# Kernel optimization log

Measured on AMD Instinct MI355X. Metric: run time of the kernel, lower is better.

## Reference

```python
import jax, jax.numpy as jnp
import numpy as np

EPS = 1e-5  # torch BatchNorm1d default eps
NH, KD, D_V = 8, 64, 128  # num_heads, key_dim, per-head value dim (attn_ratio*key_dim)


def hardswish(x):
    return x * jnp.clip(x + 3.0, 0.0, 6.0) / 6.0


def linear_bn(x, W, g, b):
    # Linear (no bias) followed by BatchNorm1d in training mode: batch stats
    # over all leading dims (torch flattens (B,N) before BN).
    y = x @ W.T
    yf = y.reshape(-1, y.shape[-1])
    mu = yf.mean(0)
    var = yf.var(0)  # biased variance, matching BN normalization
    return (y - mu) * (g / jnp.sqrt(var + EPS)) + b


def setup_inputs() -> dict:
    key = jax.random.key(0)
    ks = jax.random.split(key, 22)
    B, C, H, W, NT, D = 8, 1024, 96, 96, 60, 512
    dh = NH * D_V          # 1024
    h_kv = dh + NH * KD    # 1536
    hf = 2 * D             # 1024 (mr=2)

    def p(k, shape, s=0.02):
        return jax.random.normal(k, shape, jnp.float32) * s

    return {
        "im_emd": jax.random.normal(ks[0], (B, C, H, W), jnp.float32),
        "text_emd": jax.random.normal(ks[1], (NT, D), jnp.float32),
        "W_dc": p(ks[2], (D, C)), "g_dc": 1.0 + p(ks[3], (D,)), "b_dc": p(ks[4], (D,)),
        "W_kv": p(ks[5], (h_kv, D)), "g_kv": 1.0 + p(ks[6], (h_kv,)), "b_kv": p(ks[7], (h_kv,)),
        "W_q": p(ks[8], (NH * KD, D)), "g_q": 1.0 + p(ks[9], (NH * KD,)), "b_q": p(ks[10], (NH * KD,)),
        "W_proj": p(ks[11], (D, dh)), "g_proj": 1.0 + p(ks[12], (D,)), "b_proj": p(ks[13], (D,)),
        "biases": p(ks[14], (NH, 10000)),  # relative-position bias table (100x100 offsets)
        "W_f1": p(ks[15], (hf, D)), "g_f1": 1.0 + p(ks[16], (hf,)), "b_f1": p(ks[17], (hf,)),
        "W_f2": p(ks[18], (D, hf)), "g_f2": 1.0 + p(ks[19], (D,)), "b_f2": p(ks[20], (D,)),
    }


def _bias_idx(NT, H, W):
    # Offset table built row-major over product(range(100), range(100)) =>
    # attention_offsets[(a,b)] == 100*a + b. Text token t maps to grid point
    # (t//100, t%100); image token n to (n//W, n%W).
    t = np.arange(NT)
    n = np.arange(H * W)
    dx = np.abs(t[:, None] // 100 - n[None, :] // W)
    dy = np.abs(t[:, None] % 100 - n[None, :] % W)
    return 100 * dx + dy  # [NT, N]


def reference(im_emd, text_emd, W_dc, g_dc, b_dc, W_kv, g_kv, b_kv,
              W_q, g_q, b_q, W_proj, g_proj, b_proj, biases,
              W_f1, g_f1, b_f1, W_f2, g_f2, b_f2):
    B, C, H, W = im_emd.shape
    N = H * W
    NT, D = text_emd.shape
    dh = NH * D_V
    scale = KD ** -0.5

    # image tokens -> embed_dim
    x = im_emd.reshape(B, C, N).transpose(0, 2, 1)          # [B,N,C]
    xd = hardswish(linear_bn(x, W_dc, g_dc, b_dc))          # [B,N,D]

    # Attentioninv: text queries attend over image keys/values
    kv = linear_bn(xd, W_kv, g_kv, b_kv).reshape(B, N, NH, KD + D_V)
    k, v = kv[..., :KD], kv[..., KD:]                       # [B,N,h,64], [B,N,h,128]
    q = linear_bn(text_emd[None], W_q, g_q, b_q).reshape(NT, NH, KD)  # [NT,h,64]

    idx = jnp.asarray(_bias_idx(NT, H, W))                  # [NT,N] static
    bias = biases[:, idx]                                   # [h,NT,N] gather

    attn = jnp.einsum('thd,bnhd->bhtn', q, k) * scale + bias[None]
    attn = jax.nn.softmax(attn, axis=-1)                    # [B,h,NT,N]
    out = jnp.einsum('bhtn,bnhd->bthd', attn, v).reshape(B, NT, dh)
    out = linear_bn(hardswish(out), W_proj, g_proj, b_proj)  # [B,NT,D]

    textd = text_emd[None] + out                            # residual (broadcast)

    # ffntext: Linear_BN -> Hardswish -> Linear_BN(bn_weight_init=0) + residual
    f = hardswish(linear_bn(textd, W_f1, g_f1, b_f1))
    f = linear_bn(f, W_f2, g_f2, b_f2)
    textd = f + textd
    return textd[0]  # [NT, D]
```

## Files before the change

kernel.cpp:

```cpp
#include <hip/hip_runtime.h>
#include <hip/hip_bf16.h>
#include <stdint.h>

typedef short bf16x8 __attribute__((ext_vector_type(8)));
typedef float f32x4 __attribute__((ext_vector_type(4)));

__device__ __forceinline__ float b2f(ushort u){ return __uint_as_float(((uint32_t)u)<<16); }
__device__ __forceinline__ ushort f2b(float f){
  uint32_t u = __float_as_uint(f);
  u += 0x7fffu + ((u>>16)&1u);
  return (ushort)(u>>16);
}
__device__ __forceinline__ float hswish(float x){ return x*fminf(fmaxf(x+3.f,0.f),6.f)*(1.f/6.f); }

__device__ __forceinline__ void gll16(const void* g, void* l){
  __builtin_amdgcn_global_load_lds((const __attribute__((address_space(1))) void*)g,
                                   (__attribute__((address_space(3))) void*)l, 16, 0, 0);
}

__global__ void init_kernel(const float* __restrict__ Wdc, const float* __restrict__ Wkv,
                            ushort* __restrict__ Wdc_b, ushort* __restrict__ Wkv_b,
                            float* __restrict__ zbase){
  int i = blockIdx.x*256 + threadIdx.x;
  if (i < 8192) zbase[i] = 0.f;
  for (int j=i; j<512*1024; j+=262144) Wdc_b[j] = f2b(Wdc[j]);
  for (int j=i; j<1536*512; j+=262144) Wkv_b[j] = f2b(Wkv[j]);
}

__global__ __launch_bounds__(256) void transpose_kernel(const float* __restrict__ im, ushort* __restrict__ At){
  __shared__ float tb[64][65];
  const int b = blockIdx.z, c0 = blockIdx.y*64, n0 = blockIdx.x*64;
  const int tid = threadIdx.x;
  const int cl = tid >> 2, q = tid & 3;
  #pragma unroll
  for (int it=0; it<4; ++it){
    int nn = q*4 + it*16;
    float4 v = *(const float4*)&im[((size_t)(b*1024 + c0 + cl))*9216 + n0 + nn];
    tb[cl][nn+0]=v.x; tb[cl][nn+1]=v.y; tb[cl][nn+2]=v.z; tb[cl][nn+3]=v.w;
  }
  __syncthreads();
  const int nr = tid >> 4, c4 = (tid & 15)*4;
  #pragma unroll
  for (int ps=0; ps<4; ++ps){
    int nn = nr + ps*16;
    ushort4 u;
    u.x = f2b(tb[c4+0][nn]); u.y = f2b(tb[c4+1][nn]);
    u.z = f2b(tb[c4+2][nn]); u.w = f2b(tb[c4+3][nn]);
    *(ushort4*)&At[((size_t)(b*9216 + n0 + nn))*1024 + c0 + c4] = u;
  }
}

template<int SPLIT>
__global__ __launch_bounds__(256) void gemm_bt(
    const ushort* __restrict__ A, const ushort* __restrict__ Bm,
    ushort* __restrict__ Cm, ushort* __restrict__ Vt,
    float* __restrict__ sums, float* __restrict__ sqs,
    int NT, int N, int K)
{
  __shared__ __align__(16) ushort As[128*64];
  __shared__ __align__(16) ushort Bs[128*64];
  const int tid = threadIdx.x;
  const int l = tid & 63;
  const int w = tid >> 6;
  const int wm = w >> 1, wn = w & 1;
  const int chunk = gridDim.x >> 3;
  const int wg = (blockIdx.x & 7)*chunk + (blockIdx.x >> 3);
  const int tn = wg % NT, tm = wg / NT;
  const size_t n0 = (size_t)tn * 128;
  const size_t m0 = (size_t)tm * 128;
  const int lr = l & 15, lk = l >> 4;
  const int wbase = tid & ~63;

  const ushort* asrc[4]; const ushort* bsrc[4]; ushort* adst[4]; ushort* bdst[4];
  #pragma unroll
  for (int it=0; it<4; ++it){
    int idx = it*256 + tid;
    int row = idx >> 3, c8 = idx & 7;
    int sc8 = c8 ^ (row & 7);
    asrc[it] = A  + (m0+row)*K + sc8*8;
    bsrc[it] = Bm + (n0+row)*K + sc8*8;
    adst[it] = &As[(it*256 + wbase)*8];
    bdst[it] = &Bs[(it*256 + wbase)*8];
  }
  const int swz = (lr & 7) << 3;
  const ushort* ap0 = &As[(wm*64 + lr)*64 + ((lk*8) ^ swz)];
  const ushort* ap1 = &As[(wm*64 + lr)*64 + ((lk*8) ^ swz ^ 32)];
  const ushort* bp0 = &Bs[(wn*64 + lr)*64 + ((lk*8) ^ swz)];
  const ushort* bp1 = &Bs[(wn*64 + lr)*64 + ((lk*8) ^ swz ^ 32)];

  f32x4 acc[4][4];
  #pragma unroll
  for (int i=0;i<4;++i)
    #pragma unroll
    for (int j=0;j<4;++j) acc[i][j] = (f32x4){0.f,0.f,0.f,0.f};

  for (int kt = 0; kt < K; kt += 64) {
    #pragma unroll
    for (int it=0; it<4; ++it) {
      gll16(asrc[it] + kt, adst[it]);
      gll16(bsrc[it] + kt, bdst[it]);
    }
    __syncthreads();
    #pragma unroll
    for (int kk=0; kk<2; ++kk) {
      const ushort* ap = kk ? ap1 : ap0;
      const ushort* bp = kk ? bp1 : bp0;
      bf16x8 af[4], bfr[4];
      #pragma unroll
      for (int i=0;i<4;++i) af[i]  = *(const bf16x8*)(ap + i*1024);
      #pragma unroll
      for (int j=0;j<4;++j) bfr[j] = *(const bf16x8*)(bp + j*1024);
      #pragma unroll
      for (int i=0;i<4;++i)
        #pragma unroll
        for (int j=0;j<4;++j)
          acc[i][j] = __builtin_amdgcn_mfma_f32_16x16x32_bf16(af[i], bfr[j], acc[i][j], 0, 0, 0);
    }
    __syncthreads();
  }
  if constexpr (SPLIT==0){
    #pragma unroll
    for (int i=0;i<4;++i)
      #pragma unroll
      for (int j=0;j<4;++j)
        #pragma unroll
        for (int r=0;r<4;++r) {
          size_t row = m0 + wm*64 + i*16 + lk*4 + r;
          size_t col = n0 + wn*64 + j*16 + lr;
          Cm[row*N + col] = f2b(acc[i][j][r]);
        }
  } else {
    const int bq = (int)(m0/9216);
    const int nbase = (int)(m0 - (size_t)bq*9216);
    #pragma unroll
    for (int j=0;j<4;++j){
      int c = (int)n0 + wn*64 + j*16 + lr;
      int h = c/192, rcol = c - h*192;
      #pragma unroll
      for (int i=0;i<4;++i){
        int nrow = nbase + wm*64 + i*16 + lk*4;
        if (rcol < 64){
          ushort* kb = Cm + ((size_t)(bq*9216 + nrow))*512 + h*64 + rcol;
          #pragma unroll
          for (int r=0;r<4;++r) kb[(size_t)r*512] = f2b(acc[i][j][r]);
        } else {
          int dv = rcol - 64;
          ushort4 u;
          u.x=f2b(acc[i][j][0]); u.y=f2b(acc[i][j][1]);
          u.z=f2b(acc[i][j][2]); u.w=f2b(acc[i][j][3]);
          *(ushort4*)&Vt[((size_t)((bq*8+h)*128 + dv))*9216 + nrow] = u;
        }
      }
    }
  }
  #pragma unroll
  for (int j=0;j<4;++j){
    float cs=0.f, cq=0.f;
    #pragma unroll
    for (int i=0;i<4;++i)
      #pragma unroll
      for (int r=0;r<4;++r){ float v=acc[i][j][r]; cs+=v; cq+=v*v; }
    cs += __shfl_xor(cs,16); cs += __shfl_xor(cs,32);
    cq += __shfl_xor(cq,16); cq += __shfl_xor(cq,32);
    if (lk==0){
      int col = (int)n0 + wn*64 + j*16 + lr;
      atomicAdd(&sums[col], cs);
      atomicAdd(&sqs [col], cq);
    }
  }
}

__global__ __launch_bounds__(256) void bn_hswish(ushort* __restrict__ y,
    const float* __restrict__ ssum, const float* __restrict__ ssq,
    const float* __restrict__ g, const float* __restrict__ bb)
{
  __shared__ float sc[512], sh[512];
  const float invn = 1.f/73728.f;
  for (int i=threadIdx.x;i<512;i+=256){
    float mu = ssum[i]*invn;
    float var = ssq[i]*invn - mu*mu;
    float k = g[i]*rsqrtf(var+1e-5f);
    sc[i]=k; sh[i]=bb[i]-mu*k;
  }
  __syncthreads();
  const size_t total = (size_t)73728*512/8;
  for (size_t idx = (size_t)blockIdx.x*256+threadIdx.x; idx < total; idx += (size_t)gridDim.x*256){
    uint4 u = *(uint4*)&y[idx*8];
    ushort* up = (ushort*)&u;
    int c0 = ((int)(idx & 63))*8;
    #pragma unroll
    for (int e=0;e<8;++e){
      float x = b2f(up[e])*sc[c0+e] + sh[c0+e];
      up[e] = f2b(hswish(x));
    }
    *(uint4*)&y[idx*8] = u;
  }
}

__global__ __launch_bounds__(256) void q_gemm(const float* __restrict__ text, const float* __restrict__ Wq, float* __restrict__ qraw)
{
  __shared__ __align__(16) float xr[512];
  const int t = blockIdx.x, tid = threadIdx.x;
  for (int i=tid;i<512;i+=256) xr[i] = text[t*512+i];
  __syncthreads();
  #pragma unroll
  for (int cj=0;cj<2;++cj){
    int c = cj*256+tid;
    const float4* wp = (const float4*)(Wq + (size_t)c*512);
    const float4* xp = (const float4*)xr;
    float a=0.f;
    for (int u=0;u<128;++u){
      float4 wv = wp[u], xv = xp[u];
      a += wv.x*xv.x + wv.y*xv.y + wv.z*xv.z + wv.w*xv.w;
    }
    qraw[t*512+c]=a;
  }
}

__global__ __launch_bounds__(512) void q_bn_qh(const float* __restrict__ qraw,
                                               const float* __restrict__ g, const float* __restrict__ bb,
                                               const float* __restrict__ s2sum, const float* __restrict__ s2sq,
                                               const float* __restrict__ g_kv, const float* __restrict__ b_kv,
                                               ushort* __restrict__ Qh, float* __restrict__ cQ)
{
  const int c = threadIdx.x;
  const int h = c >> 6, d = c & 63;
  float s=0.f,q=0.f;
  for (int t=0;t<60;++t){ float v = qraw[t*512+c]; s+=v; q+=v*v; }
  float mu=s*(1.f/60.f), var=q*(1.f/60.f)-mu*mu;
  float k = g[c]*rsqrtf(var+1e-5f);
  float sh = bb[c]-mu*k;
  const float invn = 1.f/73728.f;
  float mu2 = s2sum[h*192+d]*invn;
  float var2 = s2sq[h*192+d]*invn - mu2*mu2;
  float k2 = g_kv[h*192+d]*rsqrtf(var2+1e-5f);
  const float sk = k2*0.125f;
  const float tk = (b_kv[h*192+d]-mu2*k2)*0.125f;
  for (int t=0;t<60;++t){
    float qv = qraw[t*512+c]*k+sh;
    Qh[(h*64+t)*64+d] = f2b(qv*sk);
    float contrib = qv*tk;
    #pragma unroll
    for (int o=32;o>0;o>>=1) contrib += __shfl_xor(contrib,o);
    if (d==0) cQ[h*64+t] = contrib;
  }
  for (int t=60;t<64;++t) Qh[(h*64+t)*64+d] = 0;
  if (d==0) for (int t=60;t<64;++t) cQ[h*64+t] = 0.f;
}

__global__ __launch_bounds__(256) void attn_flash(
    const ushort* __restrict__ Qh, const float* __restrict__ cQ,
    const ushort* __restrict__ Kbuf, const ushort* __restrict__ Vt,
    const float* __restrict__ biases,
    float* __restrict__ Op, float* __restrict__ Mp, float* __restrict__ Lp)
{
  __shared__ __align__(16) ushort Qs[64*72];
  __shared__ __align__(16) ushort vt[128*64];
  __shared__ __align__(16) ushort Pw[4][16*72];
  __shared__ float bias_l[600];
  __shared__ float cQs[64];
  const int tid = threadIdx.x;
  const int l = tid & 63, w = tid >> 6;
  const int lr = l & 15, lk = l >> 4;
  const int nc = blockIdx.x, h = blockIdx.y, b = blockIdx.z;
  const int bh = b*8+h;
  const int wbase = tid & ~63;
  for (int cid = tid; cid < 512; cid += 256){
    int row = cid >> 3, c8 = cid & 7;
    *(uint4*)&Qs[row*72 + c8*8] = *(const uint4*)&Qh[(size_t)(h*64+row)*64 + c8*8];
  }
  for (int i = tid; i < 600; i += 256) bias_l[i] = biases[h*10000 + nc*600 + i];
  if (tid < 64) cQs[tid] = cQ[h*64 + tid];

  const ushort* vsrc0 = Vt + (size_t)bh*128*9216 + nc*576;
  const ushort* vsrc[4]; ushort* vdst[4];
  #pragma unroll
  for (int it=0; it<4; ++it){
    int idx = it*256 + tid;
    int row = idx >> 3, c8 = idx & 7;
    int sc8 = c8 ^ (row & 7);
    vsrc[it] = vsrc0 + (size_t)row*9216 + sc8*8;
    vdst[it] = &vt[(it*256 + wbase)*8];
  }
  const int swz = (lr & 7) << 3;
  const ushort* vp0 = &vt[lr*64 + ((lk*8) ^ swz)];
  const ushort* vp1 = &vt[lr*64 + ((lk*8) ^ swz ^ 32)];
  const ushort* kchunk = Kbuf + (size_t)b*9216*512 + h*64;
  const ushort* qsp = &Qs[(w*16+lr)*72 + lk*8];
  const ushort* pwp = &Pw[w][lr*72 + lk*8];

  float m_run[4] = {-1e30f,-1e30f,-1e30f,-1e30f};
  float l_run[4] = {0.f,0.f,0.f,0.f};
  f32x4 acc_o[8];
  #pragma unroll
  for (int j=0;j<8;++j) acc_o[j] = (f32x4){0.f,0.f,0.f,0.f};
  __syncthreads();

  for (int tile=0; tile<9; ++tile){
    const int n0 = nc*576 + tile*64;
    if (tile) __syncthreads();
    #pragma unroll
    for (int it=0; it<4; ++it) gll16(vsrc[it] + tile*64, vdst[it]);
    __syncthreads();
    f32x4 sa[4];
    #pragma unroll
    for (int j=0;j<4;++j) sa[j]=(f32x4){0.f,0.f,0.f,0.f};
    const ushort* kbase = kchunk + (size_t)n0*512;
    __builtin_amdgcn_s_setprio(1);
    #pragma unroll
    for (int kk=0; kk<64; kk+=32){
      bf16x8 af = *(const bf16x8*)(qsp + kk);
      #pragma unroll
      for (int j=0;j<4;++j){
        bf16x8 bf_ = *(const bf16x8*)&kbase[(size_t)(j*16+lr)*512 + kk + lk*8];
        sa[j] = __builtin_amdgcn_mfma_f32_16x16x32_bf16(af, bf_, sa[j], 0,0,0);
      }
    }
    __builtin_amdgcn_s_setprio(0);
    float mt[4] = {-1e30f,-1e30f,-1e30f,-1e30f};
    #pragma unroll
    for (int j=0;j<4;++j){
      int n = n0 + j*16 + lr;
      int py = n/96;
      int px = n - py*96;
      int pyl = py - nc*6;
      #pragma unroll
      for (int r=0;r<4;++r){
        int t = w*16 + lk*4 + r;
        int dd = t - px; dd = dd<0?-dd:dd;
        float s = sa[j][r] + cQs[t] + bias_l[pyl*100 + dd];
        sa[j][r] = s;
        mt[r] = fmaxf(mt[r], s);
      }
    }
    #pragma unroll
    for (int r=0;r<4;++r){
      #pragma unroll
      for (int o=1;o<16;o<<=1) mt[r] = fmaxf(mt[r], __shfl_xor(mt[r], o));
      float mnew = fmaxf(m_run[r], mt[r]);
      float ef = __expf(m_run[r] - mnew);
      m_run[r] = mnew;
      l_run[r] *= ef;
      #pragma unroll
      for (int j2=0;j2<8;++j2) acc_o[j2][r] *= ef;
    }
    float rs[4] = {0.f,0.f,0.f,0.f};
    #pragma unroll
    for (int j=0;j<4;++j)
      #pragma unroll
      for (int r=0;r<4;++r){
        float pe = __expf(sa[j][r] - m_run[r]);
        rs[r] += pe;
        Pw[w][(lk*4+r)*72 + j*16 + lr] = f2b(pe);
      }
    #pragma unroll
    for (int r=0;r<4;++r){
      #pragma unroll
      for (int o=1;o<16;o<<=1) rs[r] += __shfl_xor(rs[r], o);
      l_run[r] += rs[r];
    }
    __builtin_amdgcn_s_setprio(1);
    #pragma unroll
    for (int kk=0; kk<2; ++kk){
      bf16x8 pa = *(const bf16x8*)(pwp + kk*32);
      const ushort* vp = kk ? vp1 : vp0;
      #pragma unroll
      for (int j2=0;j2<8;++j2){
        bf16x8 vb = *(const bf16x8*)(vp + j2*1024);
        acc_o[j2] = __builtin_amdgcn_mfma_f32_16x16x32_bf16(pa, vb, acc_o[j2], 0,0,0);
      }
    }
    __builtin_amdgcn_s_setprio(0);
  }
  float* ob = Op + (((size_t)nc*64 + bh)*64)*128;
  #pragma unroll
  for (int j2=0;j2<8;++j2)
    #pragma unroll
    for (int r=0;r<4;++r){
      int row = w*16 + lk*4 + r;
      ob[(size_t)row*128 + j2*16 + lr] = acc_o[j2][r];
    }
  if (lr == 0){
    #pragma unroll
    for (int r=0;r<4;++r){
      int row = w*16 + lk*4 + r;
      Mp[(nc*64+bh)*64 + row] = m_run[r];
      Lp[(nc*64+bh)*64 + row] = l_run[r];
    }
  }
}

__global__ __launch_bounds__(128) void attn_combine(
    const float* __restrict__ Op, const float* __restrict__ Mp, const float* __restrict__ Lp,
    float* __restrict__ attn_o)
{
  const int t = blockIdx.x, bh = blockIdx.y;
  const int b = bh >> 3, h = bh & 7;
  const int dv = threadIdx.x;
  float mv[16];
  float m_g = -1e30f;
  #pragma unroll
  for (int i=0;i<16;++i){ mv[i] = Mp[(i*64+bh)*64 + t]; m_g = fmaxf(m_g, mv[i]); }
  float lsum = 0.f;
  #pragma unroll
  for (int i=0;i<16;++i) lsum += Lp[(i*64+bh)*64 + t] * __expf(mv[i]-m_g);
  float o = 0.f;
  #pragma unroll
  for (int i=0;i<16;++i)
    o += Op[(((size_t)i*64 + bh)*64 + t)*128 + dv] * __expf(mv[i]-m_g);
  attn_o[(size_t)(b*60+t)*1024 + h*128 + dv] = o / lsum;
}

template<int CIN, int COUT, int MODE>
__global__ __launch_bounds__(256) void rowgemm8(
    const float* __restrict__ X, const float* __restrict__ Wt,
    const float* __restrict__ isum, const float* __restrict__ isq,
    const float* __restrict__ ig, const float* __restrict__ ib, float invn,
    const float* __restrict__ text, float* __restrict__ textd,
    float* __restrict__ out, float* __restrict__ osum, float* __restrict__ osq)
{
  __shared__ __align__(16) float xr[8][CIN];
  __shared__ float scf[CIN], shf[CIN];
  const int rb0 = blockIdx.x*8, tid = threadIdx.x;
  for (int i=tid; i<CIN; i+=256){
    int idx = (MODE==3) ? (64 + (i&127) + (i>>7)*192) : i;
    float mu = isum[idx]*invn;
    float var = isq[idx]*invn - mu*mu;
    float k = ig[idx]*rsqrtf(var+1e-5f);
    scf[i]=k; shf[i]=ib[idx]-mu*k;
  }
  __syncthreads();
  for (int i=tid; i<8*CIN; i+=256){
    int rr = i / CIN, cc = i % CIN;
    float v = X[(size_t)(rb0+rr)*CIN + cc];
    v = v*scf[cc] + shf[cc];
    if constexpr (MODE==2 || MODE==3) v = hswish(v);
    if constexpr (MODE==4){
      int t = (rb0+rr) % 60;
      v = text[t*CIN+cc] + v;
      if (blockIdx.y == 0) textd[(size_t)(rb0+rr)*CIN + cc] = v;
    }
    xr[rr][cc]=v;
  }
  __syncthreads();
  int c = blockIdx.y*256 + tid;
  const float4* wp = (const float4*)(Wt + (size_t)c*CIN);
  float a[8] = {0.f,0.f,0.f,0.f,0.f,0.f,0.f,0.f};
  for (int u=0;u<CIN/4;++u){
    float4 wv = wp[u];
    #pragma unroll
    for (int rr=0;rr<8;++rr){
      float4 xv = *(const float4*)&xr[rr][u*4];
      a[rr] += wv.x*xv.x + wv.y*xv.y + wv.z*xv.z + wv.w*xv.w;
    }
  }
  float ps=0.f, pq=0.f;
  #pragma unroll
  for (int rr=0;rr<8;++rr){
    out[(size_t)(rb0+rr)*COUT + c] = a[rr];
    ps += a[rr]; pq += a[rr]*a[rr];
  }
  atomicAdd(&osum[c], ps);
  atomicAdd(&osq [c], pq);
}

__global__ void final_out(const float* __restrict__ f2raw,
                          const float* __restrict__ ssum, const float* __restrict__ ssq,
                          const float* __restrict__ g, const float* __restrict__ bb,
                          const float* __restrict__ textd, float* __restrict__ outp)
{
  int i = blockIdx.x*256+threadIdx.x;
  if (i < 60*512){
    int c = i & 511;
    float mu = ssum[c]*(1.f/480.f);
    float var = ssq[c]*(1.f/480.f) - mu*mu;
    float k = g[c]*rsqrtf(var+1e-5f);
    outp[i] = f2raw[i]*k + (bb[c]-mu*k) + textd[i];
  }
}

extern "C" void kernel_launch(void* const* d_in, const int* in_sizes, int n_in,
                              void* d_out, int out_size, void* d_ws, size_t ws_size,
                              hipStream_t stream)
{
  (void)in_sizes; (void)n_in; (void)out_size; (void)ws_size;
  const float* im    = (const float*)d_in[0];
  const float* text  = (const float*)d_in[1];
  const float* W_dc  = (const float*)d_in[2];
  const float* g_dc  = (const float*)d_in[3];
  const float* b_dc  = (const float*)d_in[4];
  const float* W_kv  = (const float*)d_in[5];
  const float* g_kv  = (const float*)d_in[6];
  const float* b_kv  = (const float*)d_in[7];
  const float* W_q   = (const float*)d_in[8];
  const float* g_q   = (const float*)d_in[9];
  const float* b_q   = (const float*)d_in[10];
  const float* W_proj= (const float*)d_in[11];
  const float* g_proj= (const float*)d_in[12];
  const float* b_proj= (const float*)d_in[13];
  const float* biases= (const float*)d_in[14];
  const float* W_f1  = (const float*)d_in[15];
  const float* g_f1  = (const float*)d_in[16];
  const float* b_f1  = (const float*)d_in[17];
  const float* W_f2  = (const float*)d_in[18];
  const float* g_f2  = (const float*)d_in[19];
  const float* b_f2  = (const float*)d_in[20];
  float* outp = (float*)d_out;

  char* p = (char*)d_ws;
  auto alloc = [&](size_t bytes)->char*{ char* r = p; p += (bytes+255)&~(size_t)255; return r; };
  float* s1_sum = (float*)alloc(512*4);
  float* s1_sq  = (float*)alloc(512*4);
  float* s2_sum = (float*)alloc(1536*4);
  float* s2_sq  = (float*)alloc(1536*4);
  float* s3_sum = (float*)alloc(512*4);
  float* s3_sq  = (float*)alloc(512*4);
  float* s4_sum = (float*)alloc(1024*4);
  float* s4_sq  = (float*)alloc(1024*4);
  float* s5_sum = (float*)alloc(512*4);
  float* s5_sq  = (float*)alloc(512*4);
  float* zero_base = s1_sum;
  float* attn_o = (float*)alloc((size_t)480*1024*4);
  float* qraw = (float*)alloc(60*512*4);
  ushort* Qh = (ushort*)alloc((size_t)8*64*64*2);
  float* cQ = (float*)alloc(512*4);
  float* proj_raw = (float*)alloc((size_t)480*512*4);
  float* textd=(float*)alloc((size_t)480*512*4);
  float* f1_raw=(float*)alloc((size_t)480*1024*4);
  float* f2_raw=(float*)alloc((size_t)480*512*4);
  float* Op = (float*)alloc((size_t)16*64*64*128*4);
  float* Mp = (float*)alloc((size_t)16*64*64*4);
  float* Lp = (float*)alloc((size_t)16*64*64*4);
  ushort* Wdc_b = (ushort*)alloc((size_t)512*1024*2);
  ushort* Wkv_b = (ushort*)alloc((size_t)1536*512*2);
  ushort* y1 = (ushort*)alloc((size_t)73728*512*2);
  ushort* Kbuf = (ushort*)alloc((size_t)73728*512*2);
  ushort* Vt  = (ushort*)alloc((size_t)64*128*9216*2);
  ushort* At = (ushort*)alloc((size_t)73728*1024*2);

  init_kernel<<<1024,256,0,stream>>>(W_dc, W_kv, Wdc_b, Wkv_b, zero_base);
  transpose_kernel<<<dim3(144,16,8),256,0,stream>>>(im, At);
  gemm_bt<0><<<2304,256,0,stream>>>(At, Wdc_b, y1, nullptr, s1_sum, s1_sq, 4, 512, 1024);
  bn_hswish<<<2048,256,0,stream>>>(y1, s1_sum, s1_sq, g_dc, b_dc);
  gemm_bt<1><<<6912,256,0,stream>>>(y1, Wkv_b, Kbuf, Vt, s2_sum, s2_sq, 12, 1536, 512);
  q_gemm<<<60,256,0,stream>>>(text, W_q, qraw);
  q_bn_qh<<<1,512,0,stream>>>(qraw, g_q, b_q, s2_sum, s2_sq, g_kv, b_kv, Qh, cQ);
  attn_flash<<<dim3(16,8,8),256,0,stream>>>(Qh, cQ, Kbuf, Vt, biases, Op, Mp, Lp);
  attn_combine<<<dim3(60,64),128,0,stream>>>(Op, Mp, Lp, attn_o);
  rowgemm8<1024,512,3><<<dim3(60,2),256,0,stream>>>(attn_o, W_proj, s2_sum, s2_sq, g_kv, b_kv, 1.f/73728.f,
                                                    nullptr, nullptr, proj_raw, s3_sum, s3_sq);
  rowgemm8<512,1024,4><<<dim3(60,4),256,0,stream>>>(proj_raw, W_f1, s3_sum, s3_sq, g_proj, b_proj, 1.f/480.f,
                                                    text, textd, f1_raw, s4_sum, s4_sq);
  rowgemm8<1024,512,2><<<dim3(60,2),256,0,stream>>>(f1_raw, W_f2, s4_sum, s4_sq, g_f1, b_f1, 1.f/480.f,
                                                    nullptr, nullptr, f2_raw, s5_sum, s5_sq);
  final_out<<<120,256,0,stream>>>(f2_raw, s5_sum, s5_sq, g_f2, b_f2, textd, outp);
}
```

Measured before the change: 713.2 us.

## Fuse attention combine into proj GEMM, lazy softmax rescale, constexpr GEMM dims

Three changes. The GEMM dimensions become template parameters so the K loop can be fully unrolled. Flash attention now skips rescaling the running max and accumulator unless some row's tile max grows by more than 8 over the running max. The separate split-K combine kernel is removed, and the 16 partial outputs are merged while the projection rowgemm loads its inputs. This saves a launch and an intermediate write and read, but the combine is now repeated for each column block (gridDim.y=2) and exponentials can reach up to e^8 in bf16 P.

```diff
diff --git a/kernel.cpp b/kernel.cpp
--- a/kernel.cpp
+++ b/kernel.cpp
@@ -50,12 +50,11 @@
   }
 }
 
-template<int SPLIT>
+template<int SPLIT, int NT, int N, int K>
 __global__ __launch_bounds__(256) void gemm_bt(
     const ushort* __restrict__ A, const ushort* __restrict__ Bm,
     ushort* __restrict__ Cm, ushort* __restrict__ Vt,
-    float* __restrict__ sums, float* __restrict__ sqs,
-    int NT, int N, int K)
+    float* __restrict__ sums, float* __restrict__ sqs)
 {
   __shared__ __align__(16) ushort As[128*64];
   __shared__ __align__(16) ushort Bs[128*64];
@@ -94,6 +93,7 @@
     #pragma unroll
     for (int j=0;j<4;++j) acc[i][j] = (f32x4){0.f,0.f,0.f,0.f};
 
+  #pragma unroll
   for (int kt = 0; kt < K; kt += 64) {
     #pragma unroll
     for (int it=0; it<4; ++it) {
@@ -333,16 +333,23 @@
         mt[r] = fmaxf(mt[r], s);
       }
     }
+    bool ok = true;
     #pragma unroll
     for (int r=0;r<4;++r){
       #pragma unroll
       for (int o=1;o<16;o<<=1) mt[r] = fmaxf(mt[r], __shfl_xor(mt[r], o));
-      float mnew = fmaxf(m_run[r], mt[r]);
-      float ef = __expf(m_run[r] - mnew);
-      m_run[r] = mnew;
-      l_run[r] *= ef;
-      #pragma unroll
-      for (int j2=0;j2<8;++j2) acc_o[j2][r] *= ef;
+      ok = ok && (mt[r] <= m_run[r] + 8.f);
+    }
+    if (!__all(ok)){
+      #pragma unroll
+      for (int r=0;r<4;++r){
+        float mnew = fmaxf(m_run[r], mt[r]);
+        float ef = __expf(m_run[r] - mnew);
+        m_run[r] = mnew;
+        l_run[r] *= ef;
+        #pragma unroll
+        for (int j2=0;j2<8;++j2) acc_o[j2][r] *= ef;
+      }
     }
     float rs[4] = {0.f,0.f,0.f,0.f};
     #pragma unroll
@@ -388,27 +395,6 @@
       Lp[(nc*64+bh)*64 + row] = l_run[r];
     }
   }
-}
-
-__global__ __launch_bounds__(128) void attn_combine(
-    const float* __restrict__ Op, const float* __restrict__ Mp, const float* __restrict__ Lp,
-    float* __restrict__ attn_o)
-{
-  const int t = blockIdx.x, bh = blockIdx.y;
-  const int b = bh >> 3, h = bh & 7;
-  const int dv = threadIdx.x;
-  float mv[16];
-  float m_g = -1e30f;
-  #pragma unroll
-  for (int i=0;i<16;++i){ mv[i] = Mp[(i*64+bh)*64 + t]; m_g = fmaxf(m_g, mv[i]); }
-  float lsum = 0.f;
-  #pragma unroll
-  for (int i=0;i<16;++i) lsum += Lp[(i*64+bh)*64 + t] * __expf(mv[i]-m_g);
-  float o = 0.f;
-  #pragma unroll
-  for (int i=0;i<16;++i)
-    o += Op[(((size_t)i*64 + bh)*64 + t)*128 + dv] * __expf(mv[i]-m_g);
-  attn_o[(size_t)(b*60+t)*1024 + h*128 + dv] = o / lsum;
 }
 
 template<int CIN, int COUT, int MODE>
@@ -417,28 +403,65 @@
     const float* __restrict__ isum, const float* __restrict__ isq,
     const float* __restrict__ ig, const float* __restrict__ ib, float invn,
     const float* __restrict__ text, float* __restrict__ textd,
+    const float* __restrict__ Op5, const float* __restrict__ Mp5, const float* __restrict__ Lp5,
     float* __restrict__ out, float* __restrict__ osum, float* __restrict__ osq)
 {
   __shared__ __align__(16) float xr[8][CIN];
   __shared__ float scf[CIN], shf[CIN];
+  __shared__ float eW[8][8][16];
+  __shared__ float invl[8][8];
+  __shared__ int   baseRT[8][8];
   const int rb0 = blockIdx.x*8, tid = threadIdx.x;
   for (int i=tid; i<CIN; i+=256){
-    int idx = (MODE==3) ? (64 + (i&127) + (i>>7)*192) : i;
+    int idx = (MODE==5) ? (64 + (i&127) + (i>>7)*192) : i;
     float mu = isum[idx]*invn;
     float var = isq[idx]*invn - mu*mu;
     float k = ig[idx]*rsqrtf(var+1e-5f);
     scf[i]=k; shf[i]=ib[idx]-mu*k;
   }
+  if constexpr (MODE==5){
+    if (tid < 64){
+      int rr = tid >> 3, hh = tid & 7;
+      int row = rb0 + rr;
+      int bq = row / 60;
+      int t  = row - bq*60;
+      int bh = bq*8 + hh;
+      float mv[16], mg = -1e30f;
+      #pragma unroll
+      for (int i=0;i<16;++i){ mv[i] = Mp5[(i*64+bh)*64 + t]; mg = fmaxf(mg, mv[i]); }
+      float ls = 0.f;
+      #pragma unroll
+      for (int i=0;i<16;++i){
+        float e = __expf(mv[i]-mg);
+        eW[rr][hh][i] = e;
+        ls += Lp5[(i*64+bh)*64 + t]*e;
+      }
+      invl[rr][hh] = 1.f/ls;
+      baseRT[rr][hh] = (bh*64 + t)*128;
+    }
+  }
   __syncthreads();
   for (int i=tid; i<8*CIN; i+=256){
     int rr = i / CIN, cc = i % CIN;
-    float v = X[(size_t)(rb0+rr)*CIN + cc];
-    v = v*scf[cc] + shf[cc];
-    if constexpr (MODE==2 || MODE==3) v = hswish(v);
-    if constexpr (MODE==4){
-      int t = (rb0+rr) % 60;
-      v = text[t*CIN+cc] + v;
-      if (blockIdx.y == 0) textd[(size_t)(rb0+rr)*CIN + cc] = v;
+    float v;
+    if constexpr (MODE==5){
+      int hh = cc >> 7, dv = cc & 127;
+      const float* op = Op5 + baseRT[rr][hh] + dv;
+      float o = 0.f;
+      #pragma unroll
+      for (int q=0;q<16;++q) o += op[(size_t)q*524288] * eW[rr][hh][q];
+      v = o * invl[rr][hh];
+      v = v*scf[cc] + shf[cc];
+      v = hswish(v);
+    } else {
+      v = X[(size_t)(rb0+rr)*CIN + cc];
+      v = v*scf[cc] + shf[cc];
+      if constexpr (MODE==2) v = hswish(v);
+      if constexpr (MODE==4){
+        int t = (rb0+rr) % 60;
+        v = text[t*CIN+cc] + v;
+        if (blockIdx.y == 0) textd[(size_t)(rb0+rr)*CIN + cc] = v;
+      }
     }
     xr[rr][cc]=v;
   }
@@ -520,7 +543,6 @@
   float* s5_sum = (float*)alloc(512*4);
   float* s5_sq  = (float*)alloc(512*4);
   float* zero_base = s1_sum;
-  float* attn_o = (float*)alloc((size_t)480*1024*4);
   float* qraw = (float*)alloc(60*512*4);
   ushort* Qh = (ushort*)alloc((size_t)8*64*64*2);
   float* cQ = (float*)alloc(512*4);
@@ -540,18 +562,17 @@
 
   init_kernel<<<1024,256,0,stream>>>(W_dc, W_kv, Wdc_b, Wkv_b, zero_base);
   transpose_kernel<<<dim3(144,16,8),256,0,stream>>>(im, At);
-  gemm_bt<0><<<2304,256,0,stream>>>(At, Wdc_b, y1, nullptr, s1_sum, s1_sq, 4, 512, 1024);
+  gemm_bt<0,4,512,1024><<<2304,256,0,stream>>>(At, Wdc_b, y1, nullptr, s1_sum, s1_sq);
   bn_hswish<<<2048,256,0,stream>>>(y1, s1_sum, s1_sq, g_dc, b_dc);
-  gemm_bt<1><<<6912,256,0,stream>>>(y1, Wkv_b, Kbuf, Vt, s2_sum, s2_sq, 12, 1536, 512);
+  gemm_bt<1,12,1536,512><<<6912,256,0,stream>>>(y1, Wkv_b, Kbuf, Vt, s2_sum, s2_sq);
   q_gemm<<<60,256,0,stream>>>(text, W_q, qraw);
   q_bn_qh<<<1,512,0,stream>>>(qraw, g_q, b_q, s2_sum, s2_sq, g_kv, b_kv, Qh, cQ);
   attn_flash<<<dim3(16,8,8),256,0,stream>>>(Qh, cQ, Kbuf, Vt, biases, Op, Mp, Lp);
-  attn_combine<<<dim3(60,64),128,0,stream>>>(Op, Mp, Lp, attn_o);
-  rowgemm8<1024,512,3><<<dim3(60,2),256,0,stream>>>(attn_o, W_proj, s2_sum, s2_sq, g_kv, b_kv, 1.f/73728.f,
-                                                    nullptr, nullptr, proj_raw, s3_sum, s3_sq);
+  rowgemm8<1024,512,5><<<dim3(60,2),256,0,stream>>>(nullptr, W_proj, s2_sum, s2_sq, g_kv, b_kv, 1.f/73728.f,
+                                                    nullptr, nullptr, Op, Mp, Lp, proj_raw, s3_sum, s3_sq);
   rowgemm8<512,1024,4><<<dim3(60,4),256,0,stream>>>(proj_raw, W_f1, s3_sum, s3_sq, g_proj, b_proj, 1.f/480.f,
-                                                    text, textd, f1_raw, s4_sum, s4_sq);
+                                                    text, textd, nullptr, nullptr, nullptr, f1_raw, s4_sum, s4_sq);
   rowgemm8<1024,512,2><<<dim3(60,2),256,0,stream>>>(f1_raw, W_f2, s4_sum, s4_sq, g_f1, b_f1, 1.f/480.f,
-                                                    nullptr, nullptr, f2_raw, s5_sum, s5_sq);
+                                                    nullptr, nullptr, nullptr, nullptr, nullptr, f2_raw, s5_sum, s5_sq);
   final_out<<<120,256,0,stream>>>(f2_raw, s5_sum, s5_sq, g_f2, b_f2, textd, outp);
 }
```

Result: no change. 702.7 us (median of 2 runs) (-1.5%).
